# Kernel tuning notes

Hardware: AMD Instinct MI355X
Metric: run time of the kernel (lower is better)

## Reference

```python
import jax, jax.numpy as jnp
import numpy as np

C = 256


def _conv1x1(x, w, b):
    # x: [B,C,H,W], w: [O,C], b: [O] -> 1x1 conv == per-pixel linear
    return jnp.einsum('bchw,oc->bohw', x, w) + b[None, :, None, None]


def setup_inputs() -> dict:
    key = jax.random.key(0)
    ks = jax.random.split(key, 10)
    B, H, W = 4, 64, 64
    scale = 1.0 / np.sqrt(C)
    inp = {
        'F_c': jax.random.normal(ks[0], (B, C, H, W), jnp.float32),
        'F_s': jax.random.normal(ks[1], (B, C, H, W), jnp.float32),
        'w_f': jax.random.normal(ks[2], (C, C), jnp.float32) * scale,
        'b_f': jax.random.normal(ks[3], (C,), jnp.float32) * 0.01,
        'w_g': jax.random.normal(ks[4], (C, C), jnp.float32) * scale,
        'b_g': jax.random.normal(ks[5], (C,), jnp.float32) * 0.01,
        'w_h': jax.random.normal(ks[6], (C, C), jnp.float32) * scale,
        'b_h': jax.random.normal(ks[7], (C,), jnp.float32) * 0.01,
        'w_o': jax.random.normal(ks[8], (C, C), jnp.float32) * scale,
        'b_o': jax.random.normal(ks[9], (C,), jnp.float32) * 0.01,
    }
    return inp


def reference(F_c, F_s, w_f, b_f, w_g, b_g, w_h, b_h, w_o, b_o):
    b, c, h, w = F_c.shape
    Fq = _conv1x1(F_c, w_f, b_f).reshape(b, c, -1)   # [B,C,Nq]
    G = _conv1x1(F_s, w_g, b_g).reshape(b, c, -1)    # [B,C,Nk]
    Hv = _conv1x1(F_s, w_h, b_h).reshape(b, c, -1)   # [B,C,Nk]
    # S[b,i,j] = sum_c Fq[b,c,i] * G[b,c,j]; softmax over keys j
    S = jax.nn.softmax(jnp.einsum('bci,bcj->bij', Fq, G), axis=-1)
    # result[b,c,i] = sum_j Hv[b,c,j] * S[b,i,j]
    res = jnp.einsum('bcj,bij->bci', Hv, S).reshape(b, c, h, w)
    return _conv1x1(res, w_o, b_o)
```

## Files before the change

### kernel.cpp

```cpp
#include <hip/hip_runtime.h>
#include <hip/hip_bf16.h>

typedef __attribute__((ext_vector_type(4))) float f32x4;
typedef __attribute__((ext_vector_type(16))) float f32x16;
typedef __attribute__((ext_vector_type(8))) _Float16 f16x8;
typedef __attribute__((ext_vector_type(4))) _Float16 f16x4;
typedef unsigned int uint32;
typedef unsigned short ushort;

#define MFMA16F(a, b, c) __builtin_amdgcn_mfma_f32_16x16x32_f16((a), (b), (c), 0, 0, 0)
#define MFMA32F(a, b, c) __builtin_amdgcn_mfma_f32_32x32x16_f16((a), (b), (c), 0, 0, 0)

__device__ __forceinline__ uint32 pkf16(float a, float b) {
    ushort ua = __builtin_bit_cast(ushort, (_Float16)a);
    ushort ub = __builtin_bit_cast(ushort, (_Float16)b);
    return (uint32)ua | ((uint32)ub << 16);
}
__device__ __forceinline__ void gld16(const _Float16* g, _Float16* l) {
    __builtin_amdgcn_global_load_lds(
        (const __attribute__((address_space(1))) unsigned int*)g,
        (__attribute__((address_space(3))) unsigned int*)l, 16, 0, 0);
}

__global__ __launch_bounds__(256) void transpose_f16(
    const float* __restrict__ Fc, const float* __restrict__ Fs,
    _Float16* __restrict__ Xc, _Float16* __restrict__ Xs) {
    __shared__ float lds[64][65];
    const int z = blockIdx.z;
    const int b = z & 3;
    const float* src = (z < 4) ? Fc : Fs;
    _Float16* dst = (z < 4) ? Xc : Xs;
    src += (size_t)b * 256 * 4096;
    dst += (size_t)b * 4096 * 256;
    const int i0 = blockIdx.x * 64;
    const int c0 = blockIdx.y * 64;
    const int t = threadIdx.x;
    const int rq = t >> 4;
    const int q4 = (t & 15) * 4;
#pragma unroll
    for (int p = 0; p < 4; p++) {
        int r = rq + p * 16;
        float4 v = *(const float4*)(src + (size_t)(c0 + r) * 4096 + i0 + q4);
        lds[q4 + 0][r] = v.x;
        lds[q4 + 1][r] = v.y;
        lds[q4 + 2][r] = v.z;
        lds[q4 + 3][r] = v.w;
    }
    __syncthreads();
#pragma unroll
    for (int p = 0; p < 4; p++) {
        int i = rq + p * 16;
        f16x4 hv;
#pragma unroll
        for (int e = 0; e < 4; e++) hv[e] = (_Float16)lds[i][q4 + e];
        *(f16x4*)(dst + (size_t)(i0 + i) * 256 + c0 + q4) = hv;
    }
}

__global__ __launch_bounds__(256) void convert_weights(
    const float* __restrict__ wf, const float* __restrict__ wg,
    const float* __restrict__ wh, const float* __restrict__ wo,
    _Float16* __restrict__ wfh, _Float16* __restrict__ wfl,
    _Float16* __restrict__ wgh, _Float16* __restrict__ wgl,
    _Float16* __restrict__ whb, _Float16* __restrict__ wob) {
    const int t = blockIdx.x * 256 + threadIdx.x;
    const float L2E = 1.4426950408889634f;
    float sf = wf[t] * L2E;
    _Float16 hf = (_Float16)sf;
    wfh[t] = hf;
    wfl[t] = (_Float16)(sf - (float)hf);
    float sg = wg[t];
    _Float16 hg = (_Float16)sg;
    wgh[t] = hg;
    wgl[t] = (_Float16)(sg - (float)hg);
    whb[t] = (_Float16)wh[t];
    wob[t] = (_Float16)wo[t];
}

__global__ __launch_bounds__(256) void proj_qk(
    const _Float16* __restrict__ Xc, const _Float16* __restrict__ Xs,
    const _Float16* __restrict__ wfh, const _Float16* __restrict__ wfl,
    const _Float16* __restrict__ wgh, const _Float16* __restrict__ wgl,
    const float* __restrict__ bf_, const float* __restrict__ bg_,
    _Float16* __restrict__ QF, _Float16* __restrict__ KF) {
    const int y = blockIdx.y;
    const int isK = y >> 2;
    const int b = y & 3;
    const size_t bNC = (size_t)b * 4096 * 256;
    const _Float16* A = (isK ? Xs : Xc) + bNC;
    const _Float16* Bh = isK ? wgh : wfh;
    const _Float16* Bl = isK ? wgl : wfl;
    const float* bias = isK ? bg_ : bf_;
    const float bscale = isK ? 1.0f : 1.4426950408889634f;
    _Float16* Co = (isK ? KF : QF) + bNC;
    const int m0 = (blockIdx.x & 63) * 64, n0 = (blockIdx.x >> 6) * 64;
    const int l = threadIdx.x & 63, wv = threadIdx.x >> 6;
    const int g = l >> 4, l15 = l & 15;
    const int mrow = m0 + wv * 16 + l15;

    f32x4 acc[4] = {{0, 0, 0, 0}, {0, 0, 0, 0}, {0, 0, 0, 0}, {0, 0, 0, 0}};
#pragma unroll
    for (int kk = 0; kk < 8; kk++) {
        f16x8 a = *(const f16x8*)(A + (size_t)mrow * 256 + kk * 32 + g * 8);
#pragma unroll
        for (int nt = 0; nt < 4; nt++) {
            const size_t boff = (size_t)(n0 + nt * 16 + l15) * 256 + kk * 32 + g * 8;
            f16x8 bh = *(const f16x8*)(Bh + boff);
            f16x8 bl = *(const f16x8*)(Bl + boff);
            acc[nt] = MFMA16F(a, bh, acc[nt]);
            acc[nt] = MFMA16F(a, bl, acc[nt]);
        }
    }
#pragma unroll
    for (int nt = 0; nt < 4; nt++) {
        float bn = bias[n0 + nt * 16 + l15] * bscale;
#pragma unroll
        for (int r = 0; r < 4; r++) {
            int mr = m0 + wv * 16 + g * 4 + r;
            Co[(size_t)mr * 256 + n0 + nt * 16 + l15] = (_Float16)(acc[nt][r] + bn);
        }
    }
}

__global__ __launch_bounds__(256) void proj_v(
    const _Float16* __restrict__ Xs, const _Float16* __restrict__ whb,
    const float* __restrict__ bh_, _Float16* __restrict__ VF) {
    const int b = blockIdx.y;
    const size_t bNC = (size_t)b * 4096 * 256;
    const _Float16* Bp = Xs + bNC;
    _Float16* Cp = VF + bNC;
    const int m0 = (blockIdx.x & 3) * 64, n0 = (blockIdx.x >> 2) * 64;
    const int l = threadIdx.x & 63, wv = threadIdx.x >> 6;
    const int g = l >> 4, l15 = l & 15;
    const int mrow = m0 + wv * 16 + l15;

    f32x4 acc[4] = {{0, 0, 0, 0}, {0, 0, 0, 0}, {0, 0, 0, 0}, {0, 0, 0, 0}};
#pragma unroll
    for (int kk = 0; kk < 8; kk++) {
        f16x8 a = *(const f16x8*)(whb + (size_t)mrow * 256 + kk * 32 + g * 8);
#pragma unroll
        for (int nt = 0; nt < 4; nt++) {
            f16x8 bfr = *(const f16x8*)(Bp + (size_t)(n0 + nt * 16 + l15) * 256 + kk * 32 + g * 8);
            acc[nt] = MFMA16F(a, bfr, acc[nt]);
        }
    }
#pragma unroll
    for (int nt = 0; nt < 4; nt++) {
#pragma unroll
        for (int r = 0; r < 4; r++) {
            int mr = m0 + wv * 16 + g * 4 + r;
            Cp[(size_t)mr * 4096 + n0 + nt * 16 + l15] = (_Float16)(acc[nt][r] + bh_[mr]);
        }
    }
}

__global__ __launch_bounds__(512, 2) void attn_split(
    const _Float16* __restrict__ QF, const _Float16* __restrict__ KF,
    const _Float16* __restrict__ VF, _Float16* __restrict__ Opart,
    float2* __restrict__ ML) {
    __shared__ __align__(16) _Float16 Klds[2][32 * 256];
    __shared__ __align__(16) _Float16 Vt[2][256 * 40];

    const int h = blockIdx.x;
    const int grp = (h & 7) + 8 * ((h >> 3) & 1);
    const int itile = h >> 4;
    const int b = grp & 3, s = grp >> 2;

    const int tid = threadIdx.x;
    const int l = tid & 63, wv = tid >> 6;
    const int i31 = l & 31, hi = l >> 5;
    const int iwq = itile * 256 + wv * 32;
    const _Float16* Qb = QF + ((size_t)b * 4096 + iwq) * 256;
    const _Float16* Kb = KF + (size_t)b * 4096 * 256;
    const _Float16* Vb = VF + (size_t)b * 4096 * 256;

    f16x8 qf[16];
#pragma unroll
    for (int t = 0; t < 16; t++)
        qf[t] = *(const f16x8*)(Qb + (size_t)i31 * 256 + t * 16 + hi * 8);

    f32x16 acc[8];
#pragma unroll
    for (int ct = 0; ct < 8; ct++)
#pragma unroll
        for (int r = 0; r < 16; r++) acc[ct][r] = 0.0f;
    float M = -INFINITY, Lsum = 0.0f;

    const int vch = tid >> 1, vko = (tid & 1) * 16;
    const _Float16* Vsrc = Vb + (size_t)vch * 4096;

    const int jbeg = s * 1024, jend = jbeg + 1024;

    auto stageK = [&](int buf, int jj) {
        const _Float16* ks = Kb + (size_t)jj * 256;
#pragma unroll
        for (int q = 0; q < 2; q++) {
            int issue = wv * 2 + q;
            int row = issue * 2 + (l >> 5);
            int scol = ((l & 31) ^ (row & 7)) * 8;
            gld16(ks + (size_t)row * 256 + scol, &Klds[buf][issue * 512]);
        }
    };

    stageK(0, jbeg);
    {
        f16x8 va = *(const f16x8*)(Vsrc + jbeg + vko);
        f16x8 vb2 = *(const f16x8*)(Vsrc + jbeg + vko + 8);
        asm volatile("s_waitcnt vmcnt(0)" ::: "memory");
        *(f16x8*)&Vt[0][vch * 40 + vko] = va;
        *(f16x8*)&Vt[0][vch * 40 + vko + 8] = vb2;
    }
    __syncthreads();

    int cur = 0;
    for (int j0 = jbeg; j0 < jend; j0 += 32) {
        const bool pre = (j0 + 32) < jend;
        f16x8 va, vb2;
        if (pre) {
            stageK(cur ^ 1, j0 + 32);
            va = *(const f16x8*)(Vsrc + (j0 + 32) + vko);
            vb2 = *(const f16x8*)(Vsrc + (j0 + 32) + vko + 8);
        }
        f32x16 sacc;
#pragma unroll
        for (int r = 0; r < 16; r++) sacc[r] = 0.0f;
#pragma unroll
        for (int t = 0; t < 16; t++) {
            int pc = (2 * t + hi) ^ (i31 & 7);
            f16x8 kf = *(const f16x8*)&Klds[cur][i31 * 256 + pc * 8];
            sacc = MFMA32F(kf, qf[t], sacc);
        }
        float tm = sacc[0];
#pragma unroll
        for (int r = 1; r < 16; r++) tm = fmaxf(tm, sacc[r]);
        tm = fmaxf(tm, __shfl_xor(tm, 32));
        if (__any(tm - M > 8.0f)) {
            float newM = fmaxf(M, tm);
            float alpha = exp2f(M - newM);
            Lsum *= alpha;
            float ar[16];
#pragma unroll
            for (int r = 0; r < 16; r++)
                ar[r] = __shfl(alpha, (r & 3) + 8 * (r >> 2) + 4 * hi);
#pragma unroll
            for (int ct = 0; ct < 8; ct++)
#pragma unroll
                for (int r = 0; r < 16; r++) acc[ct][r] *= ar[r];
            M = newM;
        }
        float p[16], ps = 0.0f;
#pragma unroll
        for (int r = 0; r < 16; r++) {
            p[r] = exp2f(sacc[r] - M);
            ps += p[r];
        }
        Lsum += ps;
        uint32 Pq[4][2];
#pragma unroll
        for (int q = 0; q < 4; q++) {
            Pq[q][0] = pkf16(p[4 * q + 0], p[4 * q + 1]);
            Pq[q][1] = pkf16(p[4 * q + 2], p[4 * q + 3]);
        }
#pragma unroll
        for (int tp = 0; tp < 2; tp++) {
            uint32 x0 = Pq[2 * tp][0], y0 = Pq[2 * tp + 1][0];
            uint32 x1 = Pq[2 * tp][1], y1 = Pq[2 * tp + 1][1];
            asm volatile("v_permlane32_swap_b32 %0, %1" : "+v"(x0), "+v"(y0));
            asm volatile("v_permlane32_swap_b32 %0, %1" : "+v"(x1), "+v"(y1));
            union { uint32 u[4]; f16x8 v; } pa;
            pa.u[0] = x0;
            pa.u[1] = x1;
            pa.u[2] = y0;
            pa.u[3] = y1;
#pragma unroll
            for (int ct = 0; ct < 8; ct++) {
                f16x8 vf = *(const f16x8*)&Vt[cur][(ct * 32 + i31) * 40 + tp * 16 + hi * 8];
                acc[ct] = MFMA32F(pa.v, vf, acc[ct]);
            }
        }
        if (pre) {
            asm volatile("s_waitcnt vmcnt(0)" ::: "memory");
            *(f16x8*)&Vt[cur ^ 1][vch * 40 + vko] = va;
            *(f16x8*)&Vt[cur ^ 1][vch * 40 + vko + 8] = vb2;
        }
        __syncthreads();
        cur ^= 1;
    }
    float Lt = Lsum + __shfl_xor(Lsum, 32);
    float inv = 1.0f / Lt;
    float ivr[16];
#pragma unroll
    for (int r = 0; r < 16; r++)
        ivr[r] = __shfl(inv, (r & 3) + 8 * (r >> 2) + 4 * hi);
    const size_t sb = (size_t)(s * 4 + b);
    _Float16* Ob = Opart + (sb * 4096 + iwq) * 256;
#pragma unroll
    for (int ct = 0; ct < 8; ct++) {
#pragma unroll
        for (int r = 0; r < 16; r++) {
            int ir = (r & 3) + 8 * (r >> 2) + 4 * hi;
            Ob[(size_t)ir * 256 + ct * 32 + i31] = (_Float16)(acc[ct][r] * ivr[r]);
        }
    }
    if (l < 32) {
        float2 ml;
        ml.x = M;
        ml.y = Lt;
        ML[sb * 4096 + iwq + l] = ml;
    }
}

__global__ __launch_bounds__(256) void attn_combine(
    const _Float16* __restrict__ Opart, const float2* __restrict__ ML,
    _Float16* __restrict__ Rt) {
    const int b = blockIdx.y;
    const int i = blockIdx.x * 8 + (threadIdx.x >> 5);
    const int c0 = (threadIdx.x & 31) * 8;
    float m[4], lv[4];
#pragma unroll
    for (int s = 0; s < 4; s++) {
        float2 ml = ML[(size_t)(s * 4 + b) * 4096 + i];
        m[s] = ml.x;
        lv[s] = ml.y;
    }
    float Mmax = fmaxf(fmaxf(m[0], m[1]), fmaxf(m[2], m[3]));
    float w[4], denom = 0.0f;
#pragma unroll
    for (int s = 0; s < 4; s++) {
        w[s] = lv[s] * exp2f(m[s] - Mmax);
        denom += w[s];
    }
    float inv = 1.0f / denom;
    float o[8] = {0, 0, 0, 0, 0, 0, 0, 0};
#pragma unroll
    for (int s = 0; s < 4; s++) {
        float ws = w[s] * inv;
        f16x8 v = *(const f16x8*)(Opart + ((size_t)(s * 4 + b) * 4096 + i) * 256 + c0);
#pragma unroll
        for (int e = 0; e < 8; e++) o[e] += ws * (float)v[e];
    }
    f16x8 r;
#pragma unroll
    for (int e = 0; e < 8; e++) r[e] = (_Float16)o[e];
    *(f16x8*)(Rt + ((size_t)b * 4096 + i) * 256 + c0) = r;
}

__global__ __launch_bounds__(256) void out_proj(
    const _Float16* __restrict__ wob, const _Float16* __restrict__ Rt,
    const float* __restrict__ bo, float* __restrict__ Out) {
    const int b = blockIdx.y;
    const int m0 = (blockIdx.x & 3) * 64;
    const int n0 = (blockIdx.x >> 2) * 64;
    const int l = threadIdx.x & 63, wv = threadIdx.x >> 6;
    const int g = l >> 4, l15 = l & 15;
    const _Float16* Bp = Rt + (size_t)b * 4096 * 256;
    float* Ob = Out + (size_t)b * 256 * 4096;
    const int mrow = m0 + wv * 16 + l15;

    f32x4 acc[4] = {{0, 0, 0, 0}, {0, 0, 0, 0}, {0, 0, 0, 0}, {0, 0, 0, 0}};
#pragma unroll
    for (int kk = 0; kk < 8; kk++) {
        f16x8 a = *(const f16x8*)(wob + (size_t)mrow * 256 + kk * 32 + g * 8);
#pragma unroll
        for (int nt = 0; nt < 4; nt++) {
            f16x8 bfr = *(const f16x8*)(Bp + (size_t)(n0 + nt * 16 + l15) * 256 + kk * 32 + g * 8);
            acc[nt] = MFMA16F(a, bfr, acc[nt]);
        }
    }
#pragma unroll
    for (int nt = 0; nt < 4; nt++) {
#pragma unroll
        for (int r = 0; r < 4; r++) {
            int mr = m0 + wv * 16 + g * 4 + r;
            Ob[(size_t)mr * 4096 + n0 + nt * 16 + l15] = acc[nt][r] + bo[mr];
        }
    }
}

extern "C" void kernel_launch(void* const* d_in, const int* in_sizes, int n_in,
                              void* d_out, int out_size, void* d_ws, size_t ws_size,
                              hipStream_t stream) {
    const float* Fc = (const float*)d_in[0];
    const float* Fs = (const float*)d_in[1];
    const float* wf = (const float*)d_in[2];
    const float* bf_ = (const float*)d_in[3];
    const float* wg = (const float*)d_in[4];
    const float* bg = (const float*)d_in[5];
    const float* wh = (const float*)d_in[6];
    const float* bh = (const float*)d_in[7];
    const float* wo = (const float*)d_in[8];
    const float* bo = (const float*)d_in[9];
    float* Out = (float*)d_out;

    char* ws = (char*)d_ws;
    const size_t SZ = (size_t)4 * 4096 * 256 * 2;
    _Float16* QFp = (_Float16*)(ws + 0 * SZ);
    _Float16* KFp = (_Float16*)(ws + 1 * SZ);
    _Float16* VFp = (_Float16*)(ws + 2 * SZ);
    _Float16* Xc  = (_Float16*)(ws + 3 * SZ);
    _Float16* Xs  = (_Float16*)(ws + 4 * SZ);
    _Float16* Opart = (_Float16*)(ws + 5 * SZ);
    char* wsw = ws + 9 * SZ;
    _Float16* wfh = (_Float16*)(wsw + 0 * 131072);
    _Float16* wfl = (_Float16*)(wsw + 1 * 131072);
    _Float16* wgh = (_Float16*)(wsw + 2 * 131072);
    _Float16* wgl = (_Float16*)(wsw + 3 * 131072);
    _Float16* whb = (_Float16*)(wsw + 4 * 131072);
    _Float16* wob = (_Float16*)(wsw + 5 * 131072);
    float2* ML = (float2*)(wsw + 6 * 131072);
    _Float16* Rt = QFp;

    transpose_f16<<<dim3(64, 4, 8), 256, 0, stream>>>(Fc, Fs, Xc, Xs);
    convert_weights<<<dim3(256), 256, 0, stream>>>(wf, wg, wh, wo, wfh, wfl, wgh, wgl, whb, wob);
    proj_qk<<<dim3(256, 8), 256, 0, stream>>>(Xc, Xs, wfh, wfl, wgh, wgl, bf_, bg, QFp, KFp);
    proj_v<<<dim3(256, 4), 256, 0, stream>>>(Xs, whb, bh, VFp);
    attn_split<<<dim3(256), 512, 0, stream>>>(QFp, KFp, VFp, Opart, ML);
    attn_combine<<<dim3(512, 4), 256, 0, stream>>>(Opart, ML, Rt);
    out_proj<<<dim3(256, 4), 256, 0, stream>>>(wob, Rt, bo, Out);
}
```

Baseline: 332.9 us.

## Restructure attention split into 6-way key split with 16x16 MFMA tiles

Rewrites the split-attention kernel to use 16x16x32 MFMA tiles with 64-query blocks of 256 threads and a 6-way uneven key split, launching 1536 blocks instead of 256. The aim is better occupancy and load balance across CUs, with three blocks per CU and blocks mapped to XCDs. V is now single-buffered in LDS with register prefetch, and the P operand is rebuilt by lane shuffles. The combine kernel now merges 6 partials, and Opart is moved to reuse the Xc/Xs workspace region. The costs are more partial-output traffic and more shuffle overhead per tile.

```diff
diff --git a/kernel.cpp b/kernel.cpp
--- a/kernel.cpp
+++ b/kernel.cpp
@@ -2,14 +2,12 @@
 #include <hip/hip_bf16.h>
 
 typedef __attribute__((ext_vector_type(4))) float f32x4;
-typedef __attribute__((ext_vector_type(16))) float f32x16;
 typedef __attribute__((ext_vector_type(8))) _Float16 f16x8;
 typedef __attribute__((ext_vector_type(4))) _Float16 f16x4;
 typedef unsigned int uint32;
 typedef unsigned short ushort;
 
 #define MFMA16F(a, b, c) __builtin_amdgcn_mfma_f32_16x16x32_f16((a), (b), (c), 0, 0, 0)
-#define MFMA32F(a, b, c) __builtin_amdgcn_mfma_f32_32x32x16_f16((a), (b), (c), 0, 0, 0)
 
 __device__ __forceinline__ uint32 pkf16(float a, float b) {
     ushort ua = __builtin_bit_cast(ushort, (_Float16)a);
@@ -154,160 +152,176 @@
     }
 }
 
-__global__ __launch_bounds__(512, 2) void attn_split(
+__global__ __launch_bounds__(256, 3) void attn_split(
     const _Float16* __restrict__ QF, const _Float16* __restrict__ KF,
     const _Float16* __restrict__ VF, _Float16* __restrict__ Opart,
     float2* __restrict__ ML) {
     __shared__ __align__(16) _Float16 Klds[2][32 * 256];
-    __shared__ __align__(16) _Float16 Vt[2][256 * 40];
+    __shared__ __align__(16) _Float16 Vt[256 * 40];
 
     const int h = blockIdx.x;
-    const int grp = (h & 7) + 8 * ((h >> 3) & 1);
-    const int itile = h >> 4;
+    const int xcd = h & 7;
+    const int hr = h >> 3;
+    const int grp = xcd * 3 + (hr % 3);
+    const int itile = hr / 3;
     const int b = grp & 3, s = grp >> 2;
+    const int jbeg = (s < 4) ? s * 704 : 2816 + (s - 4) * 640;
+    const int ntile = (s < 4) ? 22 : 20;
 
     const int tid = threadIdx.x;
     const int l = tid & 63, wv = tid >> 6;
-    const int i31 = l & 31, hi = l >> 5;
-    const int iwq = itile * 256 + wv * 32;
-    const _Float16* Qb = QF + ((size_t)b * 4096 + iwq) * 256;
+    const int g = l >> 4, l15 = l & 15;
+    const int iw = itile * 64 + wv * 16;
+    const _Float16* Qb = QF + ((size_t)b * 4096 + iw) * 256;
     const _Float16* Kb = KF + (size_t)b * 4096 * 256;
     const _Float16* Vb = VF + (size_t)b * 4096 * 256;
 
-    f16x8 qf[16];
-#pragma unroll
-    for (int t = 0; t < 16; t++)
-        qf[t] = *(const f16x8*)(Qb + (size_t)i31 * 256 + t * 16 + hi * 8);
-
-    f32x16 acc[8];
-#pragma unroll
-    for (int ct = 0; ct < 8; ct++)
-#pragma unroll
-        for (int r = 0; r < 16; r++) acc[ct][r] = 0.0f;
+    f16x8 qf[8];
+#pragma unroll
+    for (int kk = 0; kk < 8; kk++)
+        qf[kk] = *(const f16x8*)(Qb + (size_t)l15 * 256 + kk * 32 + g * 8);
+
+    f32x4 acc[16];
+#pragma unroll
+    for (int ct = 0; ct < 16; ct++) acc[ct] = (f32x4){0, 0, 0, 0};
     float M = -INFINITY, Lsum = 0.0f;
 
-    const int vch = tid >> 1, vko = (tid & 1) * 16;
-    const _Float16* Vsrc = Vb + (size_t)vch * 4096;
-
-    const int jbeg = s * 1024, jend = jbeg + 1024;
-
-    auto stageK = [&](int buf, int jj) {
-        const _Float16* ks = Kb + (size_t)jj * 256;
-#pragma unroll
-        for (int q = 0; q < 2; q++) {
-            int issue = wv * 2 + q;
-            int row = issue * 2 + (l >> 5);
-            int scol = ((l & 31) ^ (row & 7)) * 8;
-            gld16(ks + (size_t)row * 256 + scol, &Klds[buf][issue * 512]);
-        }
-    };
-
-    stageK(0, jbeg);
-    {
-        f16x8 va = *(const f16x8*)(Vsrc + jbeg + vko);
-        f16x8 vb2 = *(const f16x8*)(Vsrc + jbeg + vko + 8);
+    const _Float16* Vsrc = Vb + (size_t)tid * 4096;
+
+    f16x8 vr0, vr1, vr2, vr3;
+#define LOADV(jj)                                      \
+    do {                                               \
+        vr0 = *(const f16x8*)(Vsrc + (jj));            \
+        vr1 = *(const f16x8*)(Vsrc + (jj) + 8);        \
+        vr2 = *(const f16x8*)(Vsrc + (jj) + 16);       \
+        vr3 = *(const f16x8*)(Vsrc + (jj) + 24);       \
+    } while (0)
+#define STAGEK(buf, jj)                                                     \
+    do {                                                                    \
+        const _Float16* ks = Kb + (size_t)(jj) * 256;                       \
+        _Float16* kd = &Klds[buf][0];                                       \
+        _Pragma("unroll") for (int q = 0; q < 4; q++) {                     \
+            int issue = wv * 4 + q;                                         \
+            int row = issue * 2 + (l >> 5);                                 \
+            int scol = ((l & 31) ^ row) * 8;                                \
+            gld16(ks + (size_t)row * 256 + scol, kd + issue * 512);         \
+        }                                                                   \
+    } while (0)
+
+    STAGEK(0, jbeg);
+    LOADV(jbeg);
+
+    int cur = 0;
+    const int r1 = l15 + 16;
+    for (int t = 0; t < ntile; t++) {
+        const int j0 = jbeg + t * 32;
         asm volatile("s_waitcnt vmcnt(0)" ::: "memory");
-        *(f16x8*)&Vt[0][vch * 40 + vko] = va;
-        *(f16x8*)&Vt[0][vch * 40 + vko + 8] = vb2;
-    }
-    __syncthreads();
-
-    int cur = 0;
-    for (int j0 = jbeg; j0 < jend; j0 += 32) {
-        const bool pre = (j0 + 32) < jend;
-        f16x8 va, vb2;
-        if (pre) {
-            stageK(cur ^ 1, j0 + 32);
-            va = *(const f16x8*)(Vsrc + (j0 + 32) + vko);
-            vb2 = *(const f16x8*)(Vsrc + (j0 + 32) + vko + 8);
-        }
-        f32x16 sacc;
-#pragma unroll
-        for (int r = 0; r < 16; r++) sacc[r] = 0.0f;
-#pragma unroll
-        for (int t = 0; t < 16; t++) {
-            int pc = (2 * t + hi) ^ (i31 & 7);
-            f16x8 kf = *(const f16x8*)&Klds[cur][i31 * 256 + pc * 8];
-            sacc = MFMA32F(kf, qf[t], sacc);
-        }
-        float tm = sacc[0];
-#pragma unroll
-        for (int r = 1; r < 16; r++) tm = fmaxf(tm, sacc[r]);
+#pragma unroll
+        for (int q = 0; q < 4; q++) {
+            f16x8 v = (q == 0) ? vr0 : (q == 1) ? vr1 : (q == 2) ? vr2 : vr3;
+            *(f16x8*)&Vt[tid * 40 + q * 8] = v;
+        }
+        __syncthreads();
+        if (t + 1 < ntile) {
+            STAGEK(cur ^ 1, j0 + 32);
+            LOADV(j0 + 32);
+        }
+        f32x4 s0e = {0, 0, 0, 0}, s0o = {0, 0, 0, 0};
+        f32x4 s1e = {0, 0, 0, 0}, s1o = {0, 0, 0, 0};
+#pragma unroll
+        for (int kk = 0; kk < 8; kk += 2) {
+            {
+                int cs = kk * 4 + g;
+                f16x8 k0 = *(const f16x8*)&Klds[cur][l15 * 256 + ((cs ^ l15) & 31) * 8];
+                f16x8 k1 = *(const f16x8*)&Klds[cur][r1 * 256 + ((cs ^ r1) & 31) * 8];
+                s0e = MFMA16F(k0, qf[kk], s0e);
+                s1e = MFMA16F(k1, qf[kk], s1e);
+            }
+            {
+                int cs = (kk + 1) * 4 + g;
+                f16x8 k0 = *(const f16x8*)&Klds[cur][l15 * 256 + ((cs ^ l15) & 31) * 8];
+                f16x8 k1 = *(const f16x8*)&Klds[cur][r1 * 256 + ((cs ^ r1) & 31) * 8];
+                s0o = MFMA16F(k0, qf[kk + 1], s0o);
+                s1o = MFMA16F(k1, qf[kk + 1], s1o);
+            }
+        }
+        f32x4 s0 = s0e + s0o;
+        f32x4 s1 = s1e + s1o;
+        float tm = fmaxf(fmaxf(fmaxf(s0[0], s0[1]), fmaxf(s0[2], s0[3])),
+                         fmaxf(fmaxf(s1[0], s1[1]), fmaxf(s1[2], s1[3])));
+        tm = fmaxf(tm, __shfl_xor(tm, 16));
         tm = fmaxf(tm, __shfl_xor(tm, 32));
         if (__any(tm - M > 8.0f)) {
             float newM = fmaxf(M, tm);
             float alpha = exp2f(M - newM);
             Lsum *= alpha;
-            float ar[16];
-#pragma unroll
-            for (int r = 0; r < 16; r++)
-                ar[r] = __shfl(alpha, (r & 3) + 8 * (r >> 2) + 4 * hi);
-#pragma unroll
-            for (int ct = 0; ct < 8; ct++)
-#pragma unroll
-                for (int r = 0; r < 16; r++) acc[ct][r] *= ar[r];
+            float ar[4];
+#pragma unroll
+            for (int r = 0; r < 4; r++) ar[r] = __shfl(alpha, g * 4 + r);
+#pragma unroll
+            for (int ct = 0; ct < 16; ct++) {
+#pragma unroll
+                for (int r = 0; r < 4; r++) acc[ct][r] *= ar[r];
+            }
             M = newM;
         }
-        float p[16], ps = 0.0f;
-#pragma unroll
-        for (int r = 0; r < 16; r++) {
-            p[r] = exp2f(sacc[r] - M);
-            ps += p[r];
-        }
-        Lsum += ps;
-        uint32 Pq[4][2];
-#pragma unroll
-        for (int q = 0; q < 4; q++) {
-            Pq[q][0] = pkf16(p[4 * q + 0], p[4 * q + 1]);
-            Pq[q][1] = pkf16(p[4 * q + 2], p[4 * q + 3]);
-        }
-#pragma unroll
-        for (int tp = 0; tp < 2; tp++) {
-            uint32 x0 = Pq[2 * tp][0], y0 = Pq[2 * tp + 1][0];
-            uint32 x1 = Pq[2 * tp][1], y1 = Pq[2 * tp + 1][1];
-            asm volatile("v_permlane32_swap_b32 %0, %1" : "+v"(x0), "+v"(y0));
-            asm volatile("v_permlane32_swap_b32 %0, %1" : "+v"(x1), "+v"(y1));
-            union { uint32 u[4]; f16x8 v; } pa;
-            pa.u[0] = x0;
-            pa.u[1] = x1;
-            pa.u[2] = y0;
-            pa.u[3] = y1;
-#pragma unroll
-            for (int ct = 0; ct < 8; ct++) {
-                f16x8 vf = *(const f16x8*)&Vt[cur][(ct * 32 + i31) * 40 + tp * 16 + hi * 8];
-                acc[ct] = MFMA32F(pa.v, vf, acc[ct]);
-            }
-        }
-        if (pre) {
-            asm volatile("s_waitcnt vmcnt(0)" ::: "memory");
-            *(f16x8*)&Vt[cur ^ 1][vch * 40 + vko] = va;
-            *(f16x8*)&Vt[cur ^ 1][vch * 40 + vko + 8] = vb2;
+        float p[8];
+#pragma unroll
+        for (int r = 0; r < 4; r++) {
+            p[r] = exp2f(s0[r] - M);
+            p[4 + r] = exp2f(s1[r] - M);
+        }
+        Lsum += p[0] + p[1] + p[2] + p[3] + p[4] + p[5] + p[6] + p[7];
+
+        uint32 pk[4];
+        pk[0] = pkf16(p[0], p[1]);
+        pk[1] = pkf16(p[2], p[3]);
+        pk[2] = pkf16(p[4], p[5]);
+        pk[3] = pkf16(p[6], p[7]);
+        const int ts = g >> 1;
+        const int s1l = l15 + ((g & 1) << 5);
+        uint32 w0a = __shfl(pk[0], s1l), w0b = __shfl(pk[2], s1l);
+        uint32 w1a = __shfl(pk[1], s1l), w1b = __shfl(pk[3], s1l);
+        uint32 w2a = __shfl(pk[0], s1l + 16), w2b = __shfl(pk[2], s1l + 16);
+        uint32 w3a = __shfl(pk[1], s1l + 16), w3b = __shfl(pk[3], s1l + 16);
+        union { uint32 u[4]; f16x8 v; } pun;
+        pun.u[0] = ts ? w0b : w0a;
+        pun.u[1] = ts ? w1b : w1a;
+        pun.u[2] = ts ? w2b : w2a;
+        pun.u[3] = ts ? w3b : w3a;
+        f16x8 pf = pun.v;
+
+#pragma unroll
+        for (int ct = 0; ct < 16; ct++) {
+            f16x8 vf = *(const f16x8*)&Vt[(ct * 16 + l15) * 40 + g * 8];
+            acc[ct] = MFMA16F(pf, vf, acc[ct]);
         }
         __syncthreads();
         cur ^= 1;
     }
-    float Lt = Lsum + __shfl_xor(Lsum, 32);
+    float Lt = Lsum + __shfl_xor(Lsum, 16);
+    Lt += __shfl_xor(Lt, 32);
     float inv = 1.0f / Lt;
-    float ivr[16];
-#pragma unroll
-    for (int r = 0; r < 16; r++)
-        ivr[r] = __shfl(inv, (r & 3) + 8 * (r >> 2) + 4 * hi);
+    float ivr[4];
+#pragma unroll
+    for (int r = 0; r < 4; r++) ivr[r] = __shfl(inv, g * 4 + r);
     const size_t sb = (size_t)(s * 4 + b);
-    _Float16* Ob = Opart + (sb * 4096 + iwq) * 256;
-#pragma unroll
-    for (int ct = 0; ct < 8; ct++) {
-#pragma unroll
-        for (int r = 0; r < 16; r++) {
-            int ir = (r & 3) + 8 * (r >> 2) + 4 * hi;
-            Ob[(size_t)ir * 256 + ct * 32 + i31] = (_Float16)(acc[ct][r] * ivr[r]);
-        }
-    }
-    if (l < 32) {
+    _Float16* Ob = Opart + (sb * 4096 + iw) * 256;
+#pragma unroll
+    for (int ct = 0; ct < 16; ct++) {
+#pragma unroll
+        for (int r = 0; r < 4; r++)
+            Ob[(size_t)(g * 4 + r) * 256 + ct * 16 + l15] =
+                (_Float16)(acc[ct][r] * ivr[r]);
+    }
+    if (g == 0) {
         float2 ml;
         ml.x = M;
         ml.y = Lt;
-        ML[sb * 4096 + iwq + l] = ml;
-    }
+        ML[sb * 4096 + iw + l15] = ml;
+    }
+#undef LOADV
+#undef STAGEK
 }
 
 __global__ __launch_bounds__(256) void attn_combine(
@@ -316,24 +330,26 @@
     const int b = blockIdx.y;
     const int i = blockIdx.x * 8 + (threadIdx.x >> 5);
     const int c0 = (threadIdx.x & 31) * 8;
-    float m[4], lv[4];
-#pragma unroll
-    for (int s = 0; s < 4; s++) {
+    float m[6], lv[6];
+#pragma unroll
+    for (int s = 0; s < 6; s++) {
         float2 ml = ML[(size_t)(s * 4 + b) * 4096 + i];
         m[s] = ml.x;
         lv[s] = ml.y;
     }
-    float Mmax = fmaxf(fmaxf(m[0], m[1]), fmaxf(m[2], m[3]));
-    float w[4], denom = 0.0f;
-#pragma unroll
-    for (int s = 0; s < 4; s++) {
+    float Mmax = m[0];
+#pragma unroll
+    for (int s = 1; s < 6; s++) Mmax = fmaxf(Mmax, m[s]);
+    float w[6], denom = 0.0f;
+#pragma unroll
+    for (int s = 0; s < 6; s++) {
         w[s] = lv[s] * exp2f(m[s] - Mmax);
         denom += w[s];
     }
     float inv = 1.0f / denom;
     float o[8] = {0, 0, 0, 0, 0, 0, 0, 0};
 #pragma unroll
-    for (int s = 0; s < 4; s++) {
+    for (int s = 0; s < 6; s++) {
         float ws = w[s] * inv;
         f16x8 v = *(const f16x8*)(Opart + ((size_t)(s * 4 + b) * 4096 + i) * 256 + c0);
 #pragma unroll
@@ -399,7 +415,7 @@
     _Float16* VFp = (_Float16*)(ws + 2 * SZ);
     _Float16* Xc  = (_Float16*)(ws + 3 * SZ);
     _Float16* Xs  = (_Float16*)(ws + 4 * SZ);
-    _Float16* Opart = (_Float16*)(ws + 5 * SZ);
+    _Float16* Opart = (_Float16*)(ws + 3 * SZ);
     char* wsw = ws + 9 * SZ;
     _Float16* wfh = (_Float16*)(wsw + 0 * 131072);
     _Float16* wfl = (_Float16*)(wsw + 1 * 131072);
@@ -414,7 +430,7 @@
     convert_weights<<<dim3(256), 256, 0, stream>>>(wf, wg, wh, wo, wfh, wfl, wgh, wgl, whb, wob);
     proj_qk<<<dim3(256, 8), 256, 0, stream>>>(Xc, Xs, wfh, wfl, wgh, wgl, bf_, bg, QFp, KFp);
     proj_v<<<dim3(256, 4), 256, 0, stream>>>(Xs, whb, bh, VFp);
-    attn_split<<<dim3(256), 512, 0, stream>>>(QFp, KFp, VFp, Opart, ML);
+    attn_split<<<dim3(1536), 256, 0, stream>>>(QFp, KFp, VFp, Opart, ML);
     attn_combine<<<dim3(512, 4), 256, 0, stream>>>(Opart, ML, Rt);
     out_proj<<<dim3(256, 4), 256, 0, stream>>>(wob, Rt, bo, Out);
 }
```

Measured after the change: 417.1 us. +25.3%, slower.
